# Optimization experiments

Measured on AMD Instinct MI355X. Metric: run time of the kernel, lower is better.

The kernel has to match this reference:

```python
import jax, jax.numpy as jnp
import numpy as np

B, L, D = 4, 816, 2048
SEP = 768            # gemma (image+text) prefix length
P_LEN = 3            # proprio tokens inside the action-expert block
N, K, H = 8, 1, 256  # heads, kv heads (GQA), head dim
G = N // K
GEMMA_MLP, ACTION_MLP = 16384, 4096
SOFTCAP = 50.0
BIG_NEG = -2.3819763e38


def rms_norm(x, scale, eps=1e-6):
    var = jnp.mean(jnp.square(x.astype(jnp.float32)), axis=-1, keepdims=True)
    normed = x * jax.lax.rsqrt(var + eps)
    return (normed * (1.0 + scale)).astype(x.dtype)


def apply_rope(x, positions, max_wavelength=10_000):
    # x: [B, T, n, H], positions: [B, T]
    head_dim = x.shape[-1]
    freq_exp = (2.0 / head_dim) * jnp.arange(head_dim // 2, dtype=jnp.float32)
    timescale = max_wavelength ** freq_exp
    radians = positions[..., None].astype(jnp.float32) / timescale[None, None, :]
    radians = radians[..., None, :]  # [B, T, 1, H/2]
    sin, cos = jnp.sin(radians), jnp.cos(radians)
    x1, x2 = jnp.split(x, 2, axis=-1)
    return jnp.concatenate([x1 * cos - x2 * sin, x2 * cos + x1 * sin], axis=-1).astype(x.dtype)


def get_qkv(xn, positions, wq, wkv):
    # wq: [N, D, H], wkv: [2, K, D, H]
    q = jnp.einsum('btd,ndh->btnh', xn, wq)
    k = jnp.einsum('bsd,kdh->bskh', xn, wkv[0])
    v = jnp.einsum('bsd,kdh->bskh', xn, wkv[1])
    q = apply_rope(q, positions) * (H ** -0.5)  # query_pre_attn_norm='rsqrt_head_dim'
    k = apply_rope(k, positions)
    return q, k, v


def geglu_ffn(x, w_gating, w_linear):
    # gemma GeGLU: w_gating [2, D, hidden], w_linear [hidden, D]
    gate = jax.nn.gelu(jnp.einsum('btd,dh->bth', x, w_gating[0]))
    act = gate * jnp.einsum('btd,dh->bth', x, w_gating[1])
    return jnp.einsum('bth,hd->btd', act, w_linear)


def setup_inputs() -> dict:
    key = jax.random.key(0)
    ks = jax.random.split(key, 16)
    s = 0.02
    x = jax.random.normal(ks[0], (B, L, D), jnp.float32)
    positions = jnp.broadcast_to(jnp.arange(L, dtype=jnp.int32), (B, L))
    # PiZero block mask: full attention within gemma prefix; proprio and action
    # blocks attend to everything before them plus themselves (mask_ar cumsum trick).
    mask_ar = np.zeros(L, dtype=np.int64)
    mask_ar[SEP] = 1
    mask_ar[SEP + P_LEN] = 1
    cm = np.cumsum(mask_ar)
    attn = cm[None, :] <= cm[:, None]  # [L_q, L_kv]
    attn_mask = jnp.asarray(np.broadcast_to(attn[None, None], (B, 1, L, L)))
    return {
        'x': x,
        'positions': positions,
        'attn_mask': attn_mask,
        'separation_idx': SEP,
        'pre_attn_scale': jnp.zeros((D,), jnp.float32),
        'pre_ffw_scale': jnp.zeros((D,), jnp.float32),
        'gq_w': jax.random.normal(ks[1], (N, D, H), jnp.float32) * s,
        'gkv_w': jax.random.normal(ks[2], (2, K, D, H), jnp.float32) * s,
        'go_w': jax.random.normal(ks[3], (N, H, D), jnp.float32) * s,
        'aq_w': jax.random.normal(ks[4], (N, D, H), jnp.float32) * s,
        'akv_w': jax.random.normal(ks[5], (2, K, D, H), jnp.float32) * s,
        'ao_w': jax.random.normal(ks[6], (N, H, D), jnp.float32) * s,
        'g_gating': jax.random.normal(ks[7], (2, D, GEMMA_MLP), jnp.float32) * s,
        'g_linear': jax.random.normal(ks[8], (GEMMA_MLP, D), jnp.float32) * s,
        'a_gating': jax.random.normal(ks[9], (2, D, ACTION_MLP), jnp.float32) * s,
        'a_linear': jax.random.normal(ks[10], (ACTION_MLP, D), jnp.float32) * s,
    }


def reference(x, positions, attn_mask, separation_idx, pre_attn_scale, pre_ffw_scale,
              gq_w, gkv_w, go_w, aq_w, akv_w, ao_w,
              g_gating, g_linear, a_gating, a_linear):
    sep = separation_idx
    xg, xa = x[:, :sep, :], x[:, sep:, :]
    # shared pre-attention RMSNorm applied to both expert streams
    ng = rms_norm(xg, pre_attn_scale)
    na = rms_norm(xa, pre_attn_scale)
    pg, pa = positions[:, :sep], positions[:, sep:]
    qg, kg, vg = get_qkv(ng, pg, gq_w, gkv_w)
    qa, ka, va = get_qkv(na, pa, aq_w, akv_w)
    # joint attention over concatenated streams
    q = jnp.concatenate([qg, qa], axis=1)   # [B, L, N, H]
    k = jnp.concatenate([kg, ka], axis=1)   # [B, L, K, H]
    v = jnp.concatenate([vg, va], axis=1)
    Bq, T = q.shape[0], q.shape[1]
    qr = q.reshape(Bq, T, K, G, H)
    logits = jnp.einsum('btkgh,bskh->bkgts', qr, k)
    logits = jnp.tanh(logits / SOFTCAP) * SOFTCAP  # attn logit softcap
    logits = jnp.where(attn_mask[:, :, None, :, :], logits, BIG_NEG)
    probs = jax.nn.softmax(logits.astype(jnp.float32), axis=-1).astype(logits.dtype)
    attn_out = jnp.einsum('bkgts,bskh->btkgh', probs, v).reshape(Bq, T, N, H)
    # per-expert output projections
    og = jnp.einsum('btnh,nhd->btd', attn_out[:, :sep], go_w)
    oa = jnp.einsum('btnh,nhd->btd', attn_out[:, sep:], ao_w)

    def post(attn_o, res, gating, lin):
        # faithful to source: final residual is mlp(norm(attn+res)) + res
        h = rms_norm(attn_o + res, pre_ffw_scale)
        return geglu_ffn(h, gating, lin) + res

    yg = post(og, xg, g_gating, g_linear)
    ya = post(oa, xa, a_gating, a_linear)
    return jnp.concatenate([yg, ya], axis=1)
```

## Files before the change

kernel.cpp:

```cpp
#include <hip/hip_runtime.h>
#include <hip/hip_bf16.h>

typedef __bf16 bfx8 __attribute__((ext_vector_type(8)));
typedef __bf16 bfx4 __attribute__((ext_vector_type(4)));
typedef float f32x4 __attribute__((ext_vector_type(4)));

#define MFMA16(a, b, c) __builtin_amdgcn_mfma_f32_16x16x32_bf16((a), (b), (c), 0, 0, 0)

__device__ __forceinline__ void gl_lds16(const __bf16* g, __bf16* l) {
  __builtin_amdgcn_global_load_lds(
      (const __attribute__((address_space(1))) unsigned int*)(const void*)g,
      (__attribute__((address_space(3))) unsigned int*)(void*)l, 16, 0, 0);
}

__device__ __forceinline__ unsigned pack_bf2(float a, float b) {
  unsigned short ua = __builtin_bit_cast(unsigned short, (__bf16)a);
  unsigned short ub = __builtin_bit_cast(unsigned short, (__bf16)b);
  return (unsigned)ua | ((unsigned)ub << 16);
}

__device__ __forceinline__ float gelu_tanh_f(float x) {
  float u = 0.7978845608028654f * (x + 0.044715f * x * x * x);
  float t;
  if (u > 10.f) t = 1.f;
  else if (u < -10.f) t = -1.f;
  else { float e = __expf(2.f * u); t = (e - 1.f) / (e + 1.f); }
  return 0.5f * x * (1.f + t);
}

__global__ __launch_bounds__(256)
void rmsnorm_kernel(const float* __restrict__ X, const float* __restrict__ X2,
                    const float* __restrict__ scale, __bf16* __restrict__ out) {
  __shared__ float wsum[4];
  const int row = blockIdx.x, tid = threadIdx.x;
  const size_t base = (size_t)row * 2048;
  f32x4 v[2];
  float ss = 0.f;
#pragma unroll
  for (int i = 0; i < 2; ++i) {
    const int idx = tid * 4 + i * 1024;
    v[i] = *(const f32x4*)(X + base + idx);
    if (X2) { f32x4 u = *(const f32x4*)(X2 + base + idx); v[i] = v[i] + u; }
#pragma unroll
    for (int j = 0; j < 4; ++j) ss += v[i][j] * v[i][j];
  }
#pragma unroll
  for (int o = 32; o > 0; o >>= 1) ss += __shfl_xor(ss, o, 64);
  if ((tid & 63) == 0) wsum[tid >> 6] = ss;
  __syncthreads();
  const float tot = wsum[0] + wsum[1] + wsum[2] + wsum[3];
  const float rs = rsqrtf(tot * (1.f / 2048.f) + 1e-6f);
#pragma unroll
  for (int i = 0; i < 2; ++i) {
    const int idx = tid * 4 + i * 1024;
    f32x4 sc = *(const f32x4*)(scale + idx);
    bfx4 ov;
#pragma unroll
    for (int j = 0; j < 4; ++j) ov[j] = (__bf16)(v[i][j] * rs * (1.f + sc[j]));
    *(bfx4*)(out + base + idx) = ov;
  }
}

__global__ __launch_bounds__(256)
void rope_bf_kernel(__bf16* __restrict__ buf, const int* __restrict__ pos,
                    int nheads, int rstride, float outscale) {
  const int row = blockIdx.x;
  const float p = (float)pos[row];
  const int total = nheads * 128;
  const size_t rbase = (size_t)row * (size_t)rstride;
  for (int idx = threadIdx.x; idx < total; idx += 256) {
    const int n = idx >> 7, i = idx & 127;
    const float ts = __expf(-(float)i * 0.071955784f);
    float sn, cs;
    __sincosf(p * ts, &sn, &cs);
    __bf16* bp = buf + rbase + n * 256 + i;
    const float x1 = (float)bp[0], x2 = (float)bp[128];
    bp[0]   = (__bf16)((x1 * cs - x2 * sn) * outscale);
    bp[128] = (__bf16)((x2 * cs + x1 * sn) * outscale);
  }
}

__global__ __launch_bounds__(256)
void rope_kernel(const float* __restrict__ in, const int* __restrict__ pos,
                 __bf16* __restrict__ outp, int nheads, float outscale) {
  const int row = blockIdx.x;
  const float p = (float)pos[row];
  const int total = nheads * 128;
  const size_t rbase = (size_t)row * (size_t)(nheads * 256);
  for (int idx = threadIdx.x; idx < total; idx += 256) {
    const int n = idx >> 7, i = idx & 127;
    const float ts = __expf(-(float)i * 0.071955784f);
    float sn, cs;
    __sincosf(p * ts, &sn, &cs);
    const float* bp = in + rbase + n * 256 + i;
    const float x1 = bp[0], x2 = bp[128];
    __bf16* ob = outp + rbase + n * 256 + i;
    ob[0]   = (__bf16)((x1 * cs - x2 * sn) * outscale);
    ob[128] = (__bf16)((x2 * cs + x1 * sn) * outscale);
  }
}

__global__ __launch_bounds__(256)
void convw_kernel(const float* __restrict__ in, __bf16* __restrict__ out,
                  int K, int headDim) {
  __shared__ __bf16 tile[64][65];
  const int tc0 = blockIdx.x * 64;
  const int tk0 = blockIdx.y * 64;
  const int tid = threadIdx.x;
  const int cchunk = tid & 15, krow = tid >> 4;
  const int c = tc0 + cchunk * 4;
  const float* colbase = in + (size_t)(c / headDim) * (size_t)K * headDim + (c % headDim);
#pragma unroll
  for (int i = 0; i < 4; ++i) {
    const int k = tk0 + krow + i * 16;
    f32x4 v = *(const f32x4*)(colbase + (size_t)k * headDim);
#pragma unroll
    for (int j = 0; j < 4; ++j) tile[cchunk * 4 + j][krow + i * 16] = (__bf16)v[j];
  }
  __syncthreads();
  const int nks = K >> 5;
#pragma unroll
  for (int s = 0; s < 2; ++s) {
    const int ch = tid + s * 256;
    const int wc = ch >> 3, wk8 = (ch & 7) * 8;
    bfx8 v;
#pragma unroll
    for (int j = 0; j < 8; ++j) v[j] = tile[wc][wk8 + j];
    const int col = tc0 + wc;
    const int kchunk = (tk0 + wk8) >> 3;
    const int cp = col >> 7, m = col & 127;
    const int ks = kchunk >> 2, lg = kchunk & 3;
    const int p = lg ^ ((m >> 1) & 3);
    *(bfx8*)(out + ((size_t)(cp * nks + ks)) * 4096 + m * 32 + p * 8) = v;
  }
}

__global__ __launch_bounds__(256, 2)
void gemm_bt2(const __bf16* __restrict__ A, const __bf16* __restrict__ Bt,
              void* __restrict__ C, void* __restrict__ C2, const void* __restrict__ Extra,
              int Mpb, int lda, int strideA, int Kd,
              int ldc, int strideC, int mbPerBatch,
              int outMode, int ldct) {
  __shared__ __align__(16) __bf16 As[2][8192];
  __shared__ __align__(16) __bf16 Bs[2][8192];
  const int tid = threadIdx.x;
  const int lane = tid & 63;
  const int wid = tid >> 6;
  const int b = blockIdx.x / mbPerBatch;
  const int row0 = (blockIdx.x % mbPerBatch) * 128;
  const int col0 = blockIdx.y * 128;
  const __bf16* Ab = A + (size_t)b * strideA;
  const size_t nks = (size_t)(Kd >> 5);
  const __bf16* Bpan0 = Bt + ((size_t)(col0 >> 7)) * nks * 4096;
  const int wm = (wid >> 1) * 64, wn = (wid & 1) * 64;
  const int qi = lane & 15, g = lane >> 4;

  const int m0 = tid >> 2, p0 = tid & 3;
  const int lg0 = p0 ^ ((m0 >> 1) & 3);
  const int m1 = m0 + 64;
  const int lg1 = p0 ^ ((m1 >> 1) & 3);
  int mr0 = row0 + m0; if (mr0 >= Mpb) mr0 = Mpb - 1;
  int mr1 = row0 + m1; if (mr1 >= Mpb) mr1 = Mpb - 1;
  const __bf16* asrc0 = Ab + (size_t)mr0 * lda + lg0 * 8;
  const __bf16* asrc1 = Ab + (size_t)mr1 * lda + lg1 * 8;
  const int nt = Kd >> 6;

  auto stage = [&](int t, int bufi) {
    const int k0 = t * 64;
    gl_lds16(asrc0 + k0, &As[bufi][tid * 8]);
    gl_lds16(asrc1 + k0, &As[bufi][(tid + 256) * 8]);
    gl_lds16(asrc0 + k0 + 32, &As[bufi][4096 + tid * 8]);
    gl_lds16(asrc1 + k0 + 32, &As[bufi][4096 + (tid + 256) * 8]);
    const __bf16* pb = Bpan0 + (size_t)(k0 >> 5) * 4096;
    gl_lds16(pb + tid * 8, &Bs[bufi][tid * 8]);
    gl_lds16(pb + (tid + 256) * 8, &Bs[bufi][(tid + 256) * 8]);
    gl_lds16(pb + 4096 + tid * 8, &Bs[bufi][4096 + tid * 8]);
    gl_lds16(pb + 4096 + (tid + 256) * 8, &Bs[bufi][4096 + (tid + 256) * 8]);
  };

  f32x4 acc[4][4];
#pragma unroll
  for (int i = 0; i < 4; ++i)
#pragma unroll
    for (int j = 0; j < 4; ++j) acc[i][j] = f32x4{0.f, 0.f, 0.f, 0.f};

  stage(0, 0);
  if (nt > 1) stage(1, 1);

  for (int t = 0; t < nt; ++t) {
    const int cur = t & 1;
    if (t + 1 < nt) asm volatile("s_waitcnt vmcnt(8)" ::: "memory");
    else            asm volatile("s_waitcnt vmcnt(0)" ::: "memory");
    __builtin_amdgcn_s_barrier();
    asm volatile("" ::: "memory");
#pragma unroll
    for (int ks = 0; ks < 2; ++ks) {
      bfx8 af[4], bf[4];
#pragma unroll
      for (int mi = 0; mi < 4; ++mi) {
        const int m = wm + mi * 16 + qi;
        const int sl = g ^ ((m >> 1) & 3);
        af[mi] = *(const bfx8*)(&As[cur][ks * 4096 + m * 32 + sl * 8]);
      }
#pragma unroll
      for (int ni = 0; ni < 4; ++ni) {
        const int n = wn + ni * 16 + qi;
        const int sl = g ^ ((n >> 1) & 3);
        bf[ni] = *(const bfx8*)(&Bs[cur][ks * 4096 + n * 32 + sl * 8]);
      }
#pragma unroll
      for (int mi = 0; mi < 4; ++mi)
#pragma unroll
        for (int ni = 0; ni < 4; ++ni)
          acc[mi][ni] = MFMA16(af[mi], bf[ni], acc[mi][ni]);
    }
    asm volatile("s_waitcnt lgkmcnt(0)" ::: "memory");
    __builtin_amdgcn_s_barrier();
    asm volatile("" ::: "memory");
    if (t + 2 < nt) stage(t + 2, cur);
  }

#pragma unroll
  for (int mi = 0; mi < 4; ++mi) {
#pragma unroll
    for (int ni = 0; ni < 4; ++ni) {
      const int col = col0 + wn + ni * 16 + qi;
      if (outMode == 5 && col >= 2304) {
        const int vcol = col - 2304;
        const int rowb = row0 + wm + mi * 16 + g * 4;
        if (rowb < Mpb) {
          bfx4 ov;
#pragma unroll
          for (int r = 0; r < 4; ++r) ov[r] = (__bf16)acc[mi][ni][r];
          *(bfx4*)((__bf16*)C2 + (size_t)b * (256 * 816) + (size_t)vcol * 816 + rowb) = ov;
        }
        continue;
      }
#pragma unroll
      for (int r = 0; r < 4; ++r) {
        const int row = row0 + wm + mi * 16 + g * 4 + r;
        if (row >= Mpb) continue;
        const float v = acc[mi][ni][r];
        if (outMode == 0) {
          ((float*)C)[(size_t)b * strideC + (size_t)row * ldc + col] = v;
        } else if (outMode == 1 || outMode == 5) {
          ((__bf16*)C)[(size_t)b * strideC + (size_t)row * ldc + col] = (__bf16)v;
        } else {
          const size_t ix = (size_t)b * strideC + (size_t)row * ldc + col;
          ((float*)C)[ix] = v + ((const float*)Extra)[ix];
        }
      }
    }
  }
  (void)ldct;
}

__global__ __launch_bounds__(256, 2)
void ffn_dual(const __bf16* __restrict__ A, const __bf16* __restrict__ Wg,
              const __bf16* __restrict__ Wa, __bf16* __restrict__ C,
              int Mpb, int lda, int strideA, int Kd,
              int ldc, int strideC, int mbPerBatch) {
  __shared__ __align__(16) __bf16 As[2][8192];
  __shared__ __align__(16) __bf16 Bs[2][8192];
  const int tid = threadIdx.x;
  const int lane = tid & 63;
  const int wid = tid >> 6;
  const int b = blockIdx.x / mbPerBatch;
  const int row0 = (blockIdx.x % mbPerBatch) * 128;
  const int col0 = blockIdx.y * 128;
  const __bf16* Ab = A + (size_t)b * strideA;
  const size_t nks = (size_t)(Kd >> 5);
  const int wm = (wid >> 1) * 64, wn = (wid & 1) * 64;
  const int qi = lane & 15, g = lane >> 4;

  const int m0 = tid >> 2, p0 = tid & 3;
  const int lg0 = p0 ^ ((m0 >> 1) & 3);
  const int m1 = m0 + 64;
  const int lg1 = p0 ^ ((m1 >> 1) & 3);
  int mr0 = row0 + m0; if (mr0 >= Mpb) mr0 = Mpb - 1;
  int mr1 = row0 + m1; if (mr1 >= Mpb) mr1 = Mpb - 1;
  const __bf16* asrc0 = Ab + (size_t)mr0 * lda + lg0 * 8;
  const __bf16* asrc1 = Ab + (size_t)mr1 * lda + lg1 * 8;
  const int nt = Kd >> 6;

  f32x4 gval[4][4];
  f32x4 acc[4][4];

#pragma unroll
  for (int pan = 0; pan < 2; ++pan) {
    const __bf16* Bpan0 = (pan ? Wa : Wg) + ((size_t)(col0 >> 7)) * nks * 4096;

    auto stage = [&](int t, int bufi) {
      const int k0 = t * 64;
      gl_lds16(asrc0 + k0, &As[bufi][tid * 8]);
      gl_lds16(asrc1 + k0, &As[bufi][(tid + 256) * 8]);
      gl_lds16(asrc0 + k0 + 32, &As[bufi][4096 + tid * 8]);
      gl_lds16(asrc1 + k0 + 32, &As[bufi][4096 + (tid + 256) * 8]);
      const __bf16* pb = Bpan0 + (size_t)(k0 >> 5) * 4096;
      gl_lds16(pb + tid * 8, &Bs[bufi][tid * 8]);
      gl_lds16(pb + (tid + 256) * 8, &Bs[bufi][(tid + 256) * 8]);
      gl_lds16(pb + 4096 + tid * 8, &Bs[bufi][4096 + tid * 8]);
      gl_lds16(pb + 4096 + (tid + 256) * 8, &Bs[bufi][4096 + (tid + 256) * 8]);
    };

#pragma unroll
    for (int i = 0; i < 4; ++i)
#pragma unroll
      for (int j = 0; j < 4; ++j) acc[i][j] = f32x4{0.f, 0.f, 0.f, 0.f};

    stage(0, 0);
    if (nt > 1) stage(1, 1);

    for (int t = 0; t < nt; ++t) {
      const int cur = t & 1;
      if (t + 1 < nt) asm volatile("s_waitcnt vmcnt(8)" ::: "memory");
      else            asm volatile("s_waitcnt vmcnt(0)" ::: "memory");
      __builtin_amdgcn_s_barrier();
      asm volatile("" ::: "memory");
#pragma unroll
      for (int ks = 0; ks < 2; ++ks) {
        bfx8 af[4], bf[4];
#pragma unroll
        for (int mi = 0; mi < 4; ++mi) {
          const int m = wm + mi * 16 + qi;
          const int sl = g ^ ((m >> 1) & 3);
          af[mi] = *(const bfx8*)(&As[cur][ks * 4096 + m * 32 + sl * 8]);
        }
#pragma unroll
        for (int ni = 0; ni < 4; ++ni) {
          const int n = wn + ni * 16 + qi;
          const int sl = g ^ ((n >> 1) & 3);
          bf[ni] = *(const bfx8*)(&Bs[cur][ks * 4096 + n * 32 + sl * 8]);
        }
#pragma unroll
        for (int mi = 0; mi < 4; ++mi)
#pragma unroll
          for (int ni = 0; ni < 4; ++ni)
            acc[mi][ni] = MFMA16(af[mi], bf[ni], acc[mi][ni]);
      }
      asm volatile("s_waitcnt lgkmcnt(0)" ::: "memory");
      __builtin_amdgcn_s_barrier();
      asm volatile("" ::: "memory");
      if (t + 2 < nt) stage(t + 2, cur);
    }

    if (pan == 0) {
#pragma unroll
      for (int i = 0; i < 4; ++i)
#pragma unroll
        for (int j = 0; j < 4; ++j)
#pragma unroll
          for (int r = 0; r < 4; ++r) gval[i][j][r] = gelu_tanh_f(acc[i][j][r]);
    }
  }

#pragma unroll
  for (int mi = 0; mi < 4; ++mi) {
#pragma unroll
    for (int ni = 0; ni < 4; ++ni) {
      const int col = col0 + wn + ni * 16 + qi;
#pragma unroll
      for (int r = 0; r < 4; ++r) {
        const int row = row0 + wm + mi * 16 + g * 4 + r;
        if (row >= Mpb) continue;
        C[(size_t)b * strideC + (size_t)row * ldc + col] =
            (__bf16)(gval[mi][ni][r] * acc[mi][ni][r]);
      }
    }
  }
}

__global__ __launch_bounds__(256, 2)
void gemm_kernel(const __bf16* __restrict__ A, const float* __restrict__ Bw,
                 void* __restrict__ C, const void* __restrict__ Extra,
                 int Mpb, int lda, int strideA,
                 int ldb, int headDim, int Kd,
                 int ldc, int strideC, int mbPerBatch,
                 int outMode, int ldct) {
  __shared__ __align__(16) __bf16 As[128 * 32];
  __shared__ __align__(16) __bf16 Bs[128 * 32];
  const int tid = threadIdx.x;
  const int lane = tid & 63;
  const int wid = tid >> 6;
  const int b = blockIdx.x / mbPerBatch;
  const int row0 = (blockIdx.x % mbPerBatch) * 128;
  const int col0 = blockIdx.y * 128;
  const __bf16* Ab = A + (size_t)b * strideA;
  const float* Bb = (headDim > 0)
      ? (Bw + (size_t)(col0 / headDim) * (size_t)Kd * headDim + (col0 % headDim))
      : (Bw + col0);
  const int wm = (wid >> 1) * 64, wn = (wid & 1) * 64;
  const int qi = lane & 15, g = lane >> 4;

  f32x4 acc[4][4];
#pragma unroll
  for (int i = 0; i < 4; ++i)
#pragma unroll
    for (int j = 0; j < 4; ++j) acc[i][j] = f32x4{0.f, 0.f, 0.f, 0.f};

  const int am = tid >> 2, ap = tid & 3;
  const int bn = tid >> 2, bc = tid & 3;

  for (int k0 = 0; k0 < Kd; k0 += 32) {
    __syncthreads();
#pragma unroll
    for (int s = 0; s < 2; ++s) {
      const int m = am + s * 64;
      int mr = row0 + m;
      if (mr >= Mpb) mr = Mpb - 1;
      const int lg = ap ^ ((m >> 1) & 3);
      bfx8 v = *(const bfx8*)(Ab + (size_t)mr * lda + k0 + lg * 8);
      *(bfx8*)(&As[m * 32 + ap * 8]) = v;
    }
#pragma unroll
    for (int s = 0; s < 2; ++s) {
      const int n = bn + s * 64;
      const float* bp = Bb + (size_t)(k0 + bc * 8) * ldb + n;
      bfx8 v;
#pragma unroll
      for (int i = 0; i < 8; ++i) v[i] = (__bf16)bp[(size_t)i * ldb];
      const int p = bc ^ ((n >> 1) & 3);
      *(bfx8*)(&Bs[n * 32 + p * 8]) = v;
    }
    __syncthreads();
    bfx8 af[4], bf[4];
#pragma unroll
    for (int mi = 0; mi < 4; ++mi) {
      const int m = wm + mi * 16 + qi;
      const int sl = g ^ ((m >> 1) & 3);
      af[mi] = *(const bfx8*)(&As[m * 32 + sl * 8]);
    }
#pragma unroll
    for (int ni = 0; ni < 4; ++ni) {
      const int n = wn + ni * 16 + qi;
      const int sl = g ^ ((n >> 1) & 3);
      bf[ni] = *(const bfx8*)(&Bs[n * 32 + sl * 8]);
    }
#pragma unroll
    for (int mi = 0; mi < 4; ++mi)
#pragma unroll
      for (int ni = 0; ni < 4; ++ni)
        acc[mi][ni] = MFMA16(af[mi], bf[ni], acc[mi][ni]);
  }

#pragma unroll
  for (int mi = 0; mi < 4; ++mi) {
#pragma unroll
    for (int ni = 0; ni < 4; ++ni) {
      const int col = col0 + wn + ni * 16 + qi;
#pragma unroll
      for (int r = 0; r < 4; ++r) {
        const int row = row0 + wm + mi * 16 + g * 4 + r;
        if (row >= Mpb) continue;
        const float v = acc[mi][ni][r];
        if (outMode == 0) {
          ((float*)C)[(size_t)b * strideC + (size_t)row * ldc + col] = v;
        } else if (outMode == 1) {
          ((__bf16*)C)[(size_t)b * strideC + (size_t)row * ldc + col] = (__bf16)v;
        } else if (outMode == 2) {
          const size_t ix = (size_t)b * strideC + (size_t)row * ldc + col;
          ((float*)C)[ix] = v + ((const float*)Extra)[ix];
        } else if (outMode == 3) {
          ((__bf16*)C)[(size_t)b * strideC + (size_t)col * ldct + row] = (__bf16)v;
        } else {
          const size_t ix = (size_t)b * strideC + (size_t)row * ldc + col;
          const float gt = (float)((const __bf16*)Extra)[ix];
          ((__bf16*)C)[ix] = (__bf16)(gelu_tanh_f(gt) * v);
        }
      }
    }
  }
}

__global__ __launch_bounds__(256, 2)
void attn_kernel(const __bf16* __restrict__ qp, const __bf16* __restrict__ kp0,
                 const __bf16* __restrict__ vt, __bf16* __restrict__ ao,
                 int qstride, int kstride) {
  __shared__ __align__(16) __bf16 Ps[4][1024];
  __shared__ float denw[4][16];
  const int tid = threadIdx.x, lane = tid & 63, wid = tid >> 6;
  const int qt = blockIdx.x, hn = blockIdx.y, b = blockIdx.z;
  const int q0 = qt * 64;
  const int qi = lane & 15, g = lane >> 4;

  int qrow = q0 + wid * 16 + qi;
  if (qrow > 815) qrow = 815;
  const int cmq = (qrow >= 768) + (qrow >= 771);
  const __bf16* qrp = qp + (size_t)(b * 816 + qrow) * qstride + hn * 256 + g * 8;
  bfx8 qf[8];
#pragma unroll
  for (int kf = 0; kf < 8; ++kf) qf[kf] = *(const bfx8*)(qrp + kf * 32);

  f32x4 oacc[16];
#pragma unroll
  for (int i = 0; i < 16; ++i) oacc[i] = f32x4{0.f, 0.f, 0.f, 0.f};
  float den = 0.f;

  const int ntiles = (q0 + 63 < 768) ? 12 : 13;
  for (int t = 0; t < ntiles; ++t) {
    const int kv0 = t * 64;
#pragma unroll
    for (int mi = 0; mi < 4; ++mi) {
      f32x4 sac = f32x4{0.f, 0.f, 0.f, 0.f};
      int srow = kv0 + mi * 16 + qi;
      if (srow > 815) srow = 815;
      const __bf16* kp = kp0 + (size_t)(b * 816 + srow) * kstride + g * 8;
#pragma unroll
      for (int kf = 0; kf < 8; ++kf) {
        bfx8 a = *(const bfx8*)(kp + kf * 32);
        sac = MFMA16(a, qf[kf], sac);
      }
      float pv[4];
#pragma unroll
      for (int r = 0; r < 4; ++r) {
        const int s = kv0 + mi * 16 + g * 4 + r;
        const float l = sac[r];
        const float e2 = __expf(l * 0.04f);
        const float capped = 50.f * (e2 - 1.f) / (e2 + 1.f);
        const int cms = (s >= 768) + (s >= 771);
        const bool ok = (s < 816) && (cms <= cmq);
        const float p = ok ? __expf(capped) : 0.f;
        den += p;
        pv[r] = p;
      }
      const unsigned lo = pack_bf2(pv[0], pv[1]);
      const unsigned hi = pack_bf2(pv[2], pv[3]);
      const int slot = 2 * mi + (g >> 1);
      const int phys = slot ^ (qi & 7);
      char* pb = (char*)&Ps[wid][0] + qi * 128 + phys * 16 + (g & 1) * 8;
      *(unsigned*)(pb) = lo;
      *(unsigned*)(pb + 4) = hi;
    }
    asm volatile("s_waitcnt lgkmcnt(0)" ::: "memory");
    bfx8 pa[2];
#pragma unroll
    for (int k2 = 0; k2 < 2; ++k2) {
      const int sl = (k2 * 4 + g) ^ (qi & 7);
      pa[k2] = *(const bfx8*)((const char*)&Ps[wid][0] + qi * 128 + sl * 16);
    }
#pragma unroll
    for (int hf = 0; hf < 16; ++hf) {
      const int h = hf * 16 + qi;
#pragma unroll
      for (int k2 = 0; k2 < 2; ++k2) {
        int s0 = kv0 + k2 * 32 + g * 8;
        if (s0 > 808) s0 = 808;
        bfx8 vb = *(const bfx8*)(vt + ((size_t)(b * 256 + h)) * 816 + s0);
        oacc[hf] = MFMA16(pa[k2], vb, oacc[hf]);
      }
    }
    asm volatile("s_waitcnt lgkmcnt(0)" ::: "memory");
  }

  den += __shfl_xor(den, 16, 64);
  den += __shfl_xor(den, 32, 64);
  if (lane < 16) denw[wid][qi] = den;
  asm volatile("s_waitcnt lgkmcnt(0)" ::: "memory");
#pragma unroll
  for (int r = 0; r < 4; ++r) {
    const int qg = q0 + wid * 16 + g * 4 + r;
    if (qg >= 816) continue;
    const float di = 1.f / denw[wid][g * 4 + r];
#pragma unroll
    for (int hf = 0; hf < 16; ++hf) {
      ao[((size_t)(b * 816 + qg)) * 2048 + hn * 256 + hf * 16 + qi] =
          (__bf16)(oacc[hf][r] * di);
    }
  }
}

extern "C" void kernel_launch(void* const* d_in, const int* in_sizes, int n_in,
                              void* d_out, int out_size, void* d_ws, size_t ws_size,
                              hipStream_t stream) {
  (void)in_sizes; (void)n_in; (void)out_size;
  const float* x      = (const float*)d_in[0];
  const int*   pos    = (const int*)d_in[1];
  const float* s_attn = (const float*)d_in[4];
  const float* s_ffw  = (const float*)d_in[5];
  const float* gq     = (const float*)d_in[6];
  const float* gkv    = (const float*)d_in[7];
  const float* go     = (const float*)d_in[8];
  const float* aq     = (const float*)d_in[9];
  const float* akv    = (const float*)d_in[10];
  const float* aow    = (const float*)d_in[11];
  const float* gg     = (const float*)d_in[12];
  const float* gl     = (const float*)d_in[13];
  const float* ag     = (const float*)d_in[14];
  const float* al     = (const float*)d_in[15];
  float* outp = (float*)d_out;
  char* ws = (char*)d_ws;
  dim3 blk(256);

  const size_t NEED_BATCH = 577437696u;
  const size_t NEED_FAST  = 423297024u;

  if (ws_size >= NEED_FAST) {
    const bool batched = (ws_size >= NEED_BATCH);
    __bf16* wQKVg = (__bf16*)(ws + 0);
    __bf16* wQKVa = (__bf16*)(ws + 10485760);
    __bf16* goT = (__bf16*)(ws + 20971520);
    __bf16* aoT = (__bf16*)(ws + 29360128);
    __bf16* ggT = (__bf16*)(ws + 37748736);
    __bf16* glT = (__bf16*)(ws + 171966464);
    __bf16* agT = (__bf16*)(ws + 239075328);
    __bf16* alT = (__bf16*)(ws + 272629760);
    __bf16* xn   = (__bf16*)(ws + 289406976);
    __bf16* qkb  = (__bf16*)(ws + 302776320);
    __bf16* vt   = (__bf16*)(ws + 317816832);
    __bf16* aob  = (__bf16*)(ws + 319488000);
    float*  ob   = (float*)(ws + 332857344);
    __bf16* hb   = (__bf16*)(ws + 359596032);
    __bf16* gate  = (__bf16*)(ws + 372965376);
    __bf16* act   = (__bf16*)(ws + 398131200);
    __bf16* act4  = (__bf16*)(ws + 473628672);
    __bf16* actA4 = (__bf16*)(ws + 575864832);

    convw_kernel<<<dim3(32, 32), blk, 0, stream>>>(gq, wQKVg, 2048, 256);
    convw_kernel<<<dim3(4, 32), blk, 0, stream>>>(gkv, wQKVg + 16 * 64 * 4096, 2048, 256);
    convw_kernel<<<dim3(4, 32), blk, 0, stream>>>(gkv + 2048 * 256, wQKVg + 18 * 64 * 4096, 2048, 256);
    convw_kernel<<<dim3(32, 32), blk, 0, stream>>>(aq, wQKVa, 2048, 256);
    convw_kernel<<<dim3(4, 32), blk, 0, stream>>>(akv, wQKVa + 16 * 64 * 4096, 2048, 256);
    convw_kernel<<<dim3(4, 32), blk, 0, stream>>>(akv + 2048 * 256, wQKVa + 18 * 64 * 4096, 2048, 256);
    convw_kernel<<<dim3(32, 32), blk, 0, stream>>>(go, goT, 2048, 2048);
    convw_kernel<<<dim3(32, 32), blk, 0, stream>>>(aow, aoT, 2048, 2048);
    convw_kernel<<<dim3(256, 32), blk, 0, stream>>>(gg, ggT, 2048, 16384);
    convw_kernel<<<dim3(256, 32), blk, 0, stream>>>(gg + (size_t)2048 * 16384, ggT + (size_t)16384 * 2048, 2048, 16384);
    convw_kernel<<<dim3(32, 256), blk, 0, stream>>>(gl, glT, 16384, 2048);
    convw_kernel<<<dim3(64, 32), blk, 0, stream>>>(ag, agT, 2048, 4096);
    convw_kernel<<<dim3(64, 32), blk, 0, stream>>>(ag + (size_t)2048 * 4096, agT + (size_t)4096 * 2048, 2048, 4096);
    convw_kernel<<<dim3(32, 64), blk, 0, stream>>>(al, alT, 4096, 2048);

    rmsnorm_kernel<<<3264, blk, 0, stream>>>(x, nullptr, s_attn, xn);

    gemm_bt2<<<dim3(24, 20), blk, 0, stream>>>(xn, wQKVg, qkb, vt, nullptr,
        768, 2048, 816 * 2048, 2048, 2304, 816 * 2304, 6, 5, 0);
    gemm_bt2<<<dim3(4, 20), blk, 0, stream>>>(xn + 768 * 2048, wQKVa, qkb + 768 * 2304, vt + 768, nullptr,
        48, 2048, 816 * 2048, 2048, 2304, 816 * 2304, 1, 5, 0);

    rope_bf_kernel<<<3264, blk, 0, stream>>>(qkb, pos, 8, 2304, 0.0625f);
    rope_bf_kernel<<<3264, blk, 0, stream>>>(qkb + 2048, pos, 1, 2304, 1.0f);

    attn_kernel<<<dim3(13, 8, 4), blk, 0, stream>>>(qkb, qkb + 2048, vt, aob, 2304, 2304);

    gemm_bt2<<<dim3(24, 16), blk, 0, stream>>>(aob, goT, ob, nullptr, nullptr,
        768, 2048, 816 * 2048, 2048, 2048, 816 * 2048, 6, 0, 0);
    gemm_bt2<<<dim3(4, 16), blk, 0, stream>>>(aob + 768 * 2048, aoT, ob + 768 * 2048, nullptr, nullptr,
        48, 2048, 816 * 2048, 2048, 2048, 816 * 2048, 1, 0, 0);

    rmsnorm_kernel<<<3264, blk, 0, stream>>>(ob, x, s_ffw, hb);

    if (batched) {
      ffn_dual<<<dim3(24, 128), blk, 0, stream>>>(hb, ggT, ggT + (size_t)16384 * 2048, act4,
          768, 2048, 816 * 2048, 2048, 16384, 768 * 16384, 6);
      gemm_bt2<<<dim3(24, 16), blk, 0, stream>>>(act4, glT, outp, nullptr, x,
          768, 16384, 768 * 16384, 16384, 2048, 816 * 2048, 6, 2, 0);
      ffn_dual<<<dim3(4, 32), blk, 0, stream>>>(hb + 768 * 2048, agT, agT + (size_t)4096 * 2048, actA4,
          48, 2048, 816 * 2048, 2048, 4096, 48 * 4096, 1);
      gemm_bt2<<<dim3(4, 16), blk, 0, stream>>>(actA4, alT, outp + 768 * 2048, nullptr, x + 768 * 2048,
          48, 4096, 48 * 4096, 4096, 2048, 816 * 2048, 1, 2, 0);
    } else {
      for (int bb = 0; bb < 4; ++bb) {
        const __bf16* hg = hb + (size_t)bb * 816 * 2048;
        float* og = outp + (size_t)bb * 816 * 2048;
        const float* xg = x + (size_t)bb * 816 * 2048;
        ffn_dual<<<dim3(6, 128), blk, 0, stream>>>(hg, ggT, ggT + (size_t)16384 * 2048, act,
            768, 2048, 0, 2048, 16384, 0, 6);
        gemm_bt2<<<dim3(6, 16), blk, 0, stream>>>(act, glT, og, nullptr, xg,
            768, 16384, 0, 16384, 2048, 0, 6, 2, 0);
        const __bf16* ha = hg + 768 * 2048;
        ffn_dual<<<dim3(1, 32), blk, 0, stream>>>(ha, agT, agT + (size_t)4096 * 2048, gate,
            48, 2048, 0, 2048, 4096, 0, 1);
        gemm_bt2<<<dim3(1, 16), blk, 0, stream>>>(gate, alT, og + 768 * 2048, nullptr, xg + 768 * 2048,
            48, 4096, 0, 4096, 2048, 0, 1, 2, 0);
      }
    }
    return;
  }

  if (ws_size < 164000000u) return;
  __bf16* xn   = (__bf16*)(ws + 0);
  float*  qf   = (float*)(ws + 13369344);
  __bf16* qbb  = (__bf16*)(ws + 40108032);
  float*  kf   = (float*)(ws + 53477376);
  __bf16* kbb  = (__bf16*)(ws + 56819712);
  __bf16* vt   = (__bf16*)(ws + 58490880);
  __bf16* aob  = (__bf16*)(ws + 60162048);
  float*  ob   = (float*)(ws + 73531392);
  __bf16* hb   = (__bf16*)(ws + 100270080);
  __bf16* gate = (__bf16*)(ws + 113639424);
  __bf16* act  = (__bf16*)(ws + 138805248);

  rmsnorm_kernel<<<3264, blk, 0, stream>>>(x, nullptr, s_attn, xn);
  gemm_kernel<<<dim3(24, 16), blk, 0, stream>>>(xn, gq, qf, nullptr,
      768, 2048, 816 * 2048, 256, 256, 2048, 2048, 816 * 2048, 6, 0, 0);
  gemm_kernel<<<dim3(4, 16), blk, 0, stream>>>(xn + 768 * 2048, aq, qf + 768 * 2048, nullptr,
      48, 2048, 816 * 2048, 256, 256, 2048, 2048, 816 * 2048, 1, 0, 0);
  gemm_kernel<<<dim3(24, 2), blk, 0, stream>>>(xn, gkv, kf, nullptr,
      768, 2048, 816 * 2048, 256, 256, 2048, 256, 816 * 256, 6, 0, 0);
  gemm_kernel<<<dim3(4, 2), blk, 0, stream>>>(xn + 768 * 2048, akv, kf + 768 * 256, nullptr,
      48, 2048, 816 * 2048, 256, 256, 2048, 256, 816 * 256, 1, 0, 0);
  gemm_kernel<<<dim3(24, 2), blk, 0, stream>>>(xn, gkv + 2048 * 256, vt, nullptr,
      768, 2048, 816 * 2048, 256, 256, 2048, 0, 256 * 816, 6, 3, 816);
  gemm_kernel<<<dim3(4, 2), blk, 0, stream>>>(xn + 768 * 2048, akv + 2048 * 256, vt + 768, nullptr,
      48, 2048, 816 * 2048, 256, 256, 2048, 0, 256 * 816, 1, 3, 816);
  rope_kernel<<<3264, blk, 0, stream>>>(qf, pos, qbb, 8, 0.0625f);
  rope_kernel<<<3264, blk, 0, stream>>>(kf, pos, kbb, 1, 1.0f);
  attn_kernel<<<dim3(13, 8, 4), blk, 0, stream>>>(qbb, kbb, vt, aob, 2048, 256);
  gemm_kernel<<<dim3(24, 16), blk, 0, stream>>>(aob, go, ob, nullptr,
      768, 2048, 816 * 2048, 2048, 0, 2048, 2048, 816 * 2048, 6, 0, 0);
  gemm_kernel<<<dim3(4, 16), blk, 0, stream>>>(aob + 768 * 2048, aow, ob + 768 * 2048, nullptr,
      48, 2048, 816 * 2048, 2048, 0, 2048, 2048, 816 * 2048, 1, 0, 0);
  rmsnorm_kernel<<<3264, blk, 0, stream>>>(ob, x, s_ffw, hb);
  for (int bb = 0; bb < 4; ++bb) {
    const __bf16* hg = hb + (size_t)bb * 816 * 2048;
    float* og = outp + (size_t)bb * 816 * 2048;
    const float* xg = x + (size_t)bb * 816 * 2048;
    gemm_kernel<<<dim3(6, 128), blk, 0, stream>>>(hg, gg, gate, nullptr,
        768, 2048, 0, 16384, 0, 2048, 16384, 0, 6, 1, 0);
    gemm_kernel<<<dim3(6, 128), blk, 0, stream>>>(hg, gg + 2048 * 16384, act, gate,
        768, 2048, 0, 16384, 0, 2048, 16384, 0, 6, 4, 0);
    gemm_kernel<<<dim3(6, 16), blk, 0, stream>>>(act, gl, og, xg,
        768, 16384, 0, 2048, 0, 16384, 2048, 0, 6, 2, 0);
    const __bf16* ha = hg + 768 * 2048;
    gemm_kernel<<<dim3(1, 32), blk, 0, stream>>>(ha, ag, gate, nullptr,
        48, 2048, 0, 4096, 0, 2048, 4096, 0, 1, 1, 0);
    gemm_kernel<<<dim3(1, 32), blk, 0, stream>>>(ha, ag + 2048 * 4096, act, gate,
        48, 2048, 0, 4096, 0, 2048, 4096, 0, 1, 4, 0);
    gemm_kernel<<<dim3(1, 16), blk, 0, stream>>>(act, al, og + 768 * 2048, xg + 768 * 2048,
        48, 4096, 0, 2048, 0, 4096, 2048, 0, 1, 2, 0);
  }
}
```

Before: 1.549 ms.

## Add 256-row, 512-thread dual-GEMM GeGLU kernel for gemma FFN up-projection

Adds a new ffn_dual256 kernel that computes a 256x128 output tile per block with 8 waves, instead of 128 rows with 4 waves, for the gating and linear projections plus the GeLU product. Each weight tile loaded into LDS is now reused across twice as many rows, which cuts global weight traffic for the large 2048x16384 up-projection. It uses a four-phase pipeline with interleaved global-to-LDS staging, explicit vmcnt waits and raised priority around the MFMA sections. The cost is 128KB of LDS per block with 512 threads, which may limit occupancy, and a grid of half as many blocks.

New measurement: 1.503 ms. 1.03x faster.

```diff
diff --git a/kernel.cpp b/kernel.cpp
--- a/kernel.cpp
+++ b/kernel.cpp
@@ -133,6 +133,136 @@
     const int p = lg ^ ((m >> 1) & 3);
     *(bfx8*)(out + ((size_t)(cp * nks + ks)) * 4096 + m * 32 + p * 8) = v;
   }
+}
+
+__global__ __launch_bounds__(512, 2)
+void ffn_dual256(const __bf16* __restrict__ A, const __bf16* __restrict__ Wg,
+                 const __bf16* __restrict__ Wa, __bf16* __restrict__ C,
+                 int Mpb, int lda, int strideA, int Kd,
+                 int ldc, int strideC, int mbPerBatch) {
+  __shared__ __align__(16) __bf16 As[2 * 2 * 8192];
+  __shared__ __align__(16) __bf16 Bs[2 * 2 * 8192];
+  const int tid = threadIdx.x;
+  const int lane = tid & 63;
+  const int wid = tid >> 6;
+  const int wr = wid >> 2;
+  const int wc = wid & 3;
+  const int qi = lane & 15, g = lane >> 4;
+  const int b = blockIdx.x / mbPerBatch;
+  const int row0 = (blockIdx.x % mbPerBatch) * 256;
+  const int col0 = blockIdx.y * 128;
+  const __bf16* Ab = A + (size_t)b * strideA;
+  const size_t nks = (size_t)(Kd >> 5);
+  const __bf16* Bgp = Wg + ((size_t)(col0 >> 7)) * nks * 4096;
+  const __bf16* Bap = Wa + ((size_t)(col0 >> 7)) * nks * 4096;
+  const int NT = Kd >> 6;
+
+  const int sm = tid >> 2, sp = tid & 3;
+  const int slg = sp ^ ((sm >> 1) & 3);
+  int r0 = row0 + sm;       if (r0 >= Mpb) r0 = Mpb - 1;
+  int r1 = row0 + 128 + sm; if (r1 >= Mpb) r1 = Mpb - 1;
+  const __bf16* asrc0 = Ab + (size_t)r0 * lda + slg * 8;
+  const __bf16* asrc1 = Ab + (size_t)r1 * lda + slg * 8;
+
+  auto stage_half = [&](int gh) {
+    if (gh >= 4 * NT) return;
+    const int t = gh >> 2, which = gh & 3;
+    const int bufi = t & 1;
+    if ((which & 1) == 0) {
+      const int h = which >> 1;
+      __bf16* dst = &As[bufi * 16384 + h * 8192];
+      const __bf16* src = (h ? asrc1 : asrc0) + t * 64;
+      gl_lds16(src, dst + tid * 8);
+      gl_lds16(src + 32, dst + 4096 + tid * 8);
+    } else {
+      const int pan = which >> 1;
+      __bf16* dst = &Bs[bufi * 16384 + pan * 8192];
+      const __bf16* src = (pan ? Bap : Bgp) + (size_t)(t * 2) * 4096 + tid * 8;
+      gl_lds16(src, dst + tid * 8);
+      gl_lds16(src + 4096, dst + 4096 + tid * 8);
+    }
+  };
+
+  f32x4 acc[2][2][4][2];
+#pragma unroll
+  for (int a0 = 0; a0 < 2; ++a0)
+#pragma unroll
+    for (int a1 = 0; a1 < 2; ++a1)
+#pragma unroll
+      for (int a2 = 0; a2 < 4; ++a2)
+#pragma unroll
+        for (int a3 = 0; a3 < 2; ++a3) acc[a0][a1][a2][a3] = f32x4{0.f, 0.f, 0.f, 0.f};
+
+  for (int gh = 0; gh < 6; ++gh) stage_half(gh);
+  asm volatile("s_waitcnt vmcnt(4)" ::: "memory");
+  __builtin_amdgcn_s_barrier();
+  asm volatile("" ::: "memory");
+
+  for (int t = 0; t < NT; ++t) {
+    const int cb = (t & 1) * 16384;
+#define FD_PHASE(MH, PAN, Q, VMC)                                          \
+    {                                                                       \
+      bfx8 af[4][2], bf[2][2];                                              \
+      _Pragma("unroll")                                                     \
+      for (int mi = 0; mi < 4; ++mi) {                                      \
+        const int m = wr * 64 + mi * 16 + qi;                               \
+        const int sl = g ^ ((m >> 1) & 3);                                  \
+        const int ba = cb + (MH) * 8192 + m * 32 + sl * 8;                  \
+        af[mi][0] = *(const bfx8*)(&As[ba]);                                \
+        af[mi][1] = *(const bfx8*)(&As[ba + 4096]);                         \
+      }                                                                     \
+      _Pragma("unroll")                                                     \
+      for (int ni = 0; ni < 2; ++ni) {                                      \
+        const int m = wc * 32 + ni * 16 + qi;                               \
+        const int sl = g ^ ((m >> 1) & 3);                                  \
+        const int bb = cb + (PAN) * 8192 + m * 32 + sl * 8;                 \
+        bf[ni][0] = *(const bfx8*)(&Bs[bb]);                                \
+        bf[ni][1] = *(const bfx8*)(&Bs[bb + 4096]);                         \
+      }                                                                     \
+      stage_half(4 * t + (Q) + 6);                                          \
+      VMC;                                                                  \
+      __builtin_amdgcn_s_barrier();                                         \
+      asm volatile("s_waitcnt lgkmcnt(0)" ::: "memory");                    \
+      __builtin_amdgcn_sched_barrier(0);                                    \
+      __builtin_amdgcn_s_setprio(1);                                        \
+      _Pragma("unroll")                                                     \
+      for (int mi = 0; mi < 4; ++mi)                                        \
+        _Pragma("unroll")                                                   \
+        for (int ni = 0; ni < 2; ++ni) {                                    \
+          acc[MH][PAN][mi][ni] =                                            \
+              MFMA16(af[mi][0], bf[ni][0], acc[MH][PAN][mi][ni]);           \
+          acc[MH][PAN][mi][ni] =                                            \
+              MFMA16(af[mi][1], bf[ni][1], acc[MH][PAN][mi][ni]);           \
+        }                                                                   \
+      __builtin_amdgcn_s_setprio(0);                                        \
+      __builtin_amdgcn_s_barrier();                                         \
+      asm volatile("" ::: "memory");                                        \
+    }
+
+    FD_PHASE(0, 0, 0, );
+    FD_PHASE(0, 1, 1, );
+    FD_PHASE(1, 0, 2, );
+    FD_PHASE(1, 1, 3,
+             if (t + 2 < NT) { asm volatile("s_waitcnt vmcnt(4)" ::: "memory"); }
+             else { asm volatile("s_waitcnt vmcnt(0)" ::: "memory"); });
+#undef FD_PHASE
+  }
+
+#pragma unroll
+  for (int mh = 0; mh < 2; ++mh)
+#pragma unroll
+    for (int mi = 0; mi < 4; ++mi)
+#pragma unroll
+      for (int ni = 0; ni < 2; ++ni) {
+        const int col = col0 + wc * 32 + ni * 16 + qi;
+#pragma unroll
+        for (int r = 0; r < 4; ++r) {
+          const int row = row0 + mh * 128 + wr * 64 + mi * 16 + g * 4 + r;
+          if (row >= Mpb) continue;
+          C[(size_t)b * strideC + (size_t)row * ldc + col] =
+              (__bf16)(gelu_tanh_f(acc[mh][0][mi][ni][r]) * acc[mh][1][mi][ni][r]);
+        }
+      }
 }
 
 __global__ __launch_bounds__(256, 2)
@@ -650,8 +780,8 @@
     rmsnorm_kernel<<<3264, blk, 0, stream>>>(ob, x, s_ffw, hb);
 
     if (batched) {
-      ffn_dual<<<dim3(24, 128), blk, 0, stream>>>(hb, ggT, ggT + (size_t)16384 * 2048, act4,
-          768, 2048, 816 * 2048, 2048, 16384, 768 * 16384, 6);
+      ffn_dual256<<<dim3(12, 128), dim3(512), 0, stream>>>(hb, ggT, ggT + (size_t)16384 * 2048, act4,
+          768, 2048, 816 * 2048, 2048, 16384, 768 * 16384, 3);
       gemm_bt2<<<dim3(24, 16), blk, 0, stream>>>(act4, glT, outp, nullptr, x,
           768, 16384, 768 * 16384, 16384, 2048, 816 * 2048, 6, 2, 0);
       ffn_dual<<<dim3(4, 32), blk, 0, stream>>>(hb + 768 * 2048, agT, agT + (size_t)4096 * 2048, actA4,
```
